# Performance work log

Measured on AMD Instinct MI355X. Metric: run time of the kernel, lower is better.

## Reference

```python
import jax, jax.numpy as jnp
import numpy as np

B, S, D, N, L, V = 4, 2048, 512, 16, 4, 256
EPS = 1e-5


def layernorm(x, g, b):
    m = x.mean(-1, keepdims=True)
    v = ((x - m) ** 2).mean(-1, keepdims=True)
    return (x - m) * jax.lax.rsqrt(v + EPS) * g + b


def ssm_layer(x, logA, Wd, bd, WB, bB, WC, bC, WDp, bDp, g, be):
    # x: (B,S,D)
    h = layernorm(x, g, be)
    delta = jax.nn.softplus(h @ Wd + bd)          # (B,S,D)
    Bi = h @ WB + bB                              # (B,S,N)
    Ci = h @ WC + bC                              # (B,S,N)
    A = -jnp.exp(logA)                            # (D,N)

    def step(state, inp):
        d_t, b_t, c_t, h_t = inp                  # (B,D),(B,N),(B,N),(B,D)
        dA = jnp.exp(d_t[:, :, None] * A)         # (B,D,N)
        state = dA * state + (d_t * h_t)[:, :, None] * b_t[:, None, :]
        y_t = jnp.einsum('bdn,bn->bd', state, c_t)
        return state, y_t

    xs = (jnp.moveaxis(delta, 1, 0), jnp.moveaxis(Bi, 1, 0),
          jnp.moveaxis(Ci, 1, 0), jnp.moveaxis(h, 1, 0))
    init = jnp.zeros((x.shape[0], x.shape[2], logA.shape[-1]), x.dtype)
    _, ys = jax.lax.scan(step, init, xs)
    y = jnp.moveaxis(ys, 0, 1)                    # (B,S,D)
    return x + y + h @ WDp + bDp


def setup_inputs() -> dict:
    key = jax.random.key(0)
    ks = jax.random.split(key, 12)
    s = 0.02
    byte_ids = jax.random.randint(ks[0], (B, S), 0, 256)
    emb_byte = jax.random.normal(ks[1], (V, D), jnp.float32) * s
    emb_pos = jax.random.normal(ks[2], (S, D), jnp.float32) * s
    logA = jnp.tile(jnp.log(jnp.linspace(1.0, N, N, dtype=jnp.float32)), (L, D, 1))
    Wd = jax.random.normal(ks[3], (L, D, D), jnp.float32) * s
    bd = jnp.zeros((L, D), jnp.float32)
    WB = jax.random.normal(ks[4], (L, D, N), jnp.float32) * s
    bB = jnp.zeros((L, N), jnp.float32)
    WC = jax.random.normal(ks[5], (L, D, N), jnp.float32) * s
    bC = jnp.zeros((L, N), jnp.float32)
    WDp = jax.random.normal(ks[6], (L, D, D), jnp.float32) * s
    bDp = jnp.zeros((L, D), jnp.float32)
    gamma = jnp.ones((L, D), jnp.float32)
    beta = jnp.zeros((L, D), jnp.float32)
    Wh = jax.random.normal(ks[7], (D, V), jnp.float32) * s
    bh = jnp.zeros((V,), jnp.float32)
    return {'byte_ids': byte_ids, 'emb_byte': emb_byte, 'emb_pos': emb_pos,
            'logA': logA, 'Wd': Wd, 'bd': bd, 'WB': WB, 'bB': bB,
            'WC': WC, 'bC': bC, 'WDp': WDp, 'bDp': bDp,
            'gamma': gamma, 'beta': beta, 'Wh': Wh, 'bh': bh}


def reference(byte_ids, emb_byte, emb_pos, logA, Wd, bd, WB, bB, WC, bC,
              WDp, bDp, gamma, beta, Wh, bh):
    S_ = byte_ids.shape[1]
    h = emb_byte[byte_ids] + emb_pos[:S_]
    for l in range(Wd.shape[0]):
        h = ssm_layer(h, logA[l], Wd[l], bd[l], WB[l], bB[l], WC[l], bC[l],
                      WDp[l], bDp[l], gamma[l], beta[l])
    return h @ Wh + bh                            # (B,S,256) logits
```

## Files before the change

kernel.cpp:

```cpp
#include <hip/hip_runtime.h>
#include <math.h>

#define BB 4
#define SS 2048
#define DD 512
#define NN 16
#define LL 4
#define VV 256
#define CC 64
#define TT (SS / CC)
#define EPSL 1e-5f
#define MM (BB * SS)
#define KI 16
#define LPAD 528

typedef __bf16 bf16;
typedef __attribute__((ext_vector_type(8))) __bf16 bf16x8;
typedef __attribute__((ext_vector_type(4))) __bf16 bf16x4;
typedef __attribute__((ext_vector_type(4))) float f32x4;


#define GLD_LDS(g, l) \
    __builtin_amdgcn_global_load_lds((__attribute__((address_space(1))) void*)(void*)(g), \
                                     (__attribute__((address_space(3))) void*)(l), 16, 0, 0)

__device__ __forceinline__ void ln_row_write(float4 v0, float4 v1, int lane, size_t row,
                                             const float* __restrict__ gamma,
                                             const float* __restrict__ beta,
                                             float* HN, bf16* HNb) {
    float s = v0.x + v0.y + v0.z + v0.w + v1.x + v1.y + v1.z + v1.w;
    float q = v0.x * v0.x + v0.y * v0.y + v0.z * v0.z + v0.w * v0.w +
              v1.x * v1.x + v1.y * v1.y + v1.z * v1.z + v1.w * v1.w;
#pragma unroll
    for (int o = 1; o < 64; o <<= 1) {
        s += __shfl_xor(s, o);
        q += __shfl_xor(q, o);
    }
    float m = s * (1.0f / DD);
    float var = q * (1.0f / DD) - m * m;
    float rs = rsqrtf(var + EPSL);
    float4 g0 = *(const float4*)(gamma + lane * 4);
    float4 g1 = *(const float4*)(gamma + 256 + lane * 4);
    float4 b0 = *(const float4*)(beta + lane * 4);
    float4 b1 = *(const float4*)(beta + 256 + lane * 4);
    float4 o0, o1;
    o0.x = (v0.x - m) * rs * g0.x + b0.x;
    o0.y = (v0.y - m) * rs * g0.y + b0.y;
    o0.z = (v0.z - m) * rs * g0.z + b0.z;
    o0.w = (v0.w - m) * rs * g0.w + b0.w;
    o1.x = (v1.x - m) * rs * g1.x + b1.x;
    o1.y = (v1.y - m) * rs * g1.y + b1.y;
    o1.z = (v1.z - m) * rs * g1.z + b1.z;
    o1.w = (v1.w - m) * rs * g1.w + b1.w;
    float* hr = HN + row * DD;
    *(float4*)(hr + lane * 4) = o0;
    *(float4*)(hr + 256 + lane * 4) = o1;
    size_t pb = (size_t)(row >> 4) * 8192 + (size_t)(lane >> 3) * 512 +
                (size_t)((lane & 7) >> 1) * 128 + (row & 15) * 8 + (lane & 1) * 4;
    bf16x4 p0 = {(bf16)o0.x, (bf16)o0.y, (bf16)o0.z, (bf16)o0.w};
    bf16x4 p1 = {(bf16)o1.x, (bf16)o1.y, (bf16)o1.z, (bf16)o1.w};
    *(bf16x4*)(HNb + pb) = p0;
    *(bf16x4*)(HNb + pb + 8 * 512) = p1;
}

__global__ void embed_ln(const int* __restrict__ ids,
                         const float* __restrict__ eb,
                         const float* __restrict__ ep,
                         const float* __restrict__ gamma,
                         const float* __restrict__ beta,
                         float* __restrict__ X, float* HN, bf16* HNb) {
    int wave = threadIdx.x >> 6;
    int lane = threadIdx.x & 63;
    size_t row = blockIdx.x * 4 + wave;
    int s = (int)(row & (SS - 1));
    int id = ids[row];
    const float* ebr = eb + (size_t)id * DD;
    const float* epr = ep + (size_t)s * DD;
    float4 e0 = *(const float4*)(ebr + lane * 4);
    float4 e1 = *(const float4*)(ebr + 256 + lane * 4);
    float4 p0 = *(const float4*)(epr + lane * 4);
    float4 p1 = *(const float4*)(epr + 256 + lane * 4);
    float4 v0 = {e0.x + p0.x, e0.y + p0.y, e0.z + p0.z, e0.w + p0.w};
    float4 v1 = {e1.x + p1.x, e1.y + p1.y, e1.z + p1.z, e1.w + p1.w};
    *(float4*)(X + row * DD + lane * 4) = v0;
    *(float4*)(X + row * DD + 256 + lane * 4) = v1;
    ln_row_write(v0, v1, lane, row, gamma, beta, HN, HNb);
}

__global__ __launch_bounds__(256) void convert_weights(const float* __restrict__ Wd,
                                                       const float* __restrict__ WDp,
                                                       const float* __restrict__ Wh,
                                                       bf16* __restrict__ WtP) {
    __shared__ float slab[512 * 17];
    int blk = blockIdx.x;
    const float* src;
    int nsrc, col0;
    bf16* dst;
    if (blk < 256) {
        int l = blk >> 6, tile = blk & 63;
        src = (tile < 32) ? (Wd + (size_t)l * DD * DD) : (WDp + (size_t)l * DD * DD);
        col0 = (tile & 31) * 16;
        nsrc = DD;
        dst = WtP + ((size_t)l * 64 + tile) * 8192;
    } else {
        int tile = blk - 256;
        src = Wh;
        col0 = tile * 16;
        nsrc = VV;
        dst = WtP + (size_t)(256 + tile) * 8192;
    }
    int tid = threadIdx.x;
    int kr = tid >> 2, cq = tid & 3;
#pragma unroll
    for (int i = 0; i < 8; i++) {
        int k = i * 64 + kr;
        float4 v = *(const float4*)(src + (size_t)k * nsrc + col0 + cq * 4);
        slab[k * 17 + cq * 4 + 0] = v.x;
        slab[k * 17 + cq * 4 + 1] = v.y;
        slab[k * 17 + cq * 4 + 2] = v.z;
        slab[k * 17 + cq * 4 + 3] = v.w;
    }
    __syncthreads();
#pragma unroll
    for (int it = 0; it < 4; it++) {
        int c = it * 256 + tid;
        int ki = c >> 6, fq = (c >> 4) & 3, fm = c & 15;
        int k0 = ki * 32 + fq * 8;
        bf16x8 v;
#pragma unroll
        for (int e = 0; e < 8; e++) v[e] = (bf16)slab[(k0 + e) * 17 + fm];
        *(bf16x8*)(dst + (size_t)c * 8) = v;
    }
}

template <int MODE, int NT>
__global__ __launch_bounds__(256, 8) void gemm_pack(const bf16* __restrict__ Ap,
                                                    const bf16* __restrict__ Bp,
                                                    const float* __restrict__ bias,
                                                    const float* __restrict__ bias2,
                                                    const float* __restrict__ Xres,
                                                    float* __restrict__ O1,
                                                    float* __restrict__ O2, int Nout) {
    __shared__ bf16 As[4 * 512];
    __shared__ bf16 Bs[4 * 512];
    const int tid = threadIdx.x, wave = tid >> 6, lane = tid & 63;
    const int lin = blockIdx.x;
    const int xcd = lin & 7, i4 = lin >> 3;
    const int ms = xcd * 16 + (i4 & 15);
    const int nb = i4 >> 4;

    const bf16* gA = Ap + ((size_t)ms * 4 + wave) * 8192 + lane * 8;
    const bf16* gB = Bp + ((size_t)nb * 4 + wave) * 8192 + lane * 8;
    bf16* lA = As + wave * 512;
    bf16* lB = Bs + wave * 512;

    const int fa0 = (wave >> 1) * 2, fb0 = (wave & 1) * 2;

    f32x4 acc[2][2];
#pragma unroll
    for (int i = 0; i < 2; i++)
#pragma unroll
        for (int j = 0; j < 2; j++) acc[i][j] = (f32x4){0.f, 0.f, 0.f, 0.f};

    for (int ki = 0; ki < KI; ki++) {
        GLD_LDS(gA + ki * 512, lA);
        GLD_LDS(gB + ki * 512, lB);
        __syncthreads();
        bf16x8 af[2], bfr[2];
#pragma unroll
        for (int i = 0; i < 2; i++) af[i] = *(const bf16x8*)(As + (fa0 + i) * 512 + lane * 8);
#pragma unroll
        for (int j = 0; j < 2; j++) bfr[j] = *(const bf16x8*)(Bs + (fb0 + j) * 512 + lane * 8);
#pragma unroll
        for (int i = 0; i < 2; i++)
#pragma unroll
            for (int j = 0; j < 2; j++)
                acc[i][j] = __builtin_amdgcn_mfma_f32_16x16x32_bf16(af[i], bfr[j], acc[i][j], 0, 0, 0);
        __syncthreads();
    }

    const int fm = lane & 15, fq = lane >> 4;
#pragma unroll
    for (int i = 0; i < 2; i++) {
#pragma unroll
        for (int j = 0; j < 2; j++) {
            int col = (nb * 4 + fb0 + j) * 16 + fm;
#pragma unroll
            for (int r = 0; r < 4; r++) {
                int row = (ms * 4 + fa0 + i) * 16 + fq * 4 + r;
                float v = acc[i][j][r];
                if (MODE == 0) {
                    O1[(size_t)row * Nout + col] = v + bias[col];
                } else {
                    if (col < DD) {
                        v += bias[col];
                        v = fmaxf(v, 0.0f) + log1pf(__expf(-fabsf(v)));
                        O1[(size_t)row * DD + col] = v;
                    } else {
                        int c = col - DD;
                        O2[(size_t)row * DD + c] = v + bias2[c] + Xres[(size_t)row * DD + c];
                    }
                }
            }
        }
    }
}

__global__ __launch_bounds__(512) void scan1bc(const float* __restrict__ DEL,
                                               const float* __restrict__ HN,
                                               const float* __restrict__ WB,
                                               const float* __restrict__ bB,
                                               const float* __restrict__ WC,
                                               const float* __restrict__ bC,
                                               const float* __restrict__ logA,
                                               float* __restrict__ P,
                                               float* __restrict__ LSt,
                                               float* __restrict__ BIo,
                                               float* __restrict__ CIo) {
    __shared__ float hn[32 * LPAD];
    __shared__ float bis[32 * 16], cis[32 * 16];
    int b = blockIdx.x / CC, c = blockIdx.x % CC;
    size_t row0 = (size_t)b * SS + c * TT;
    const float* hsrc = HN + row0 * DD;
    for (int v = threadIdx.x; v < 4096; v += 512) {
        int t = v >> 7, qd = v & 127;
        float4 x = *(const float4*)(hsrc + (size_t)t * DD + qd * 4);
        *(float4*)(hn + t * LPAD + qd * 4) = x;
    }
    __syncthreads();
    {
        int t = threadIdx.x >> 4, col = threadIdx.x & 15;
        float aB = 0.0f, aC = 0.0f;
        const float* hr = hn + t * LPAD;
#pragma unroll 8
        for (int k = 0; k < DD; k++) {
            float h = hr[k];
            aB = fmaf(h, WB[k * NN + col], aB);
            aC = fmaf(h, WC[k * NN + col], aC);
        }
        aB += bB[col];
        aC += bC[col];
        bis[threadIdx.x] = aB;
        cis[threadIdx.x] = aC;
        BIo[row0 * NN + threadIdx.x] = aB;
        CIo[row0 * NN + threadIdx.x] = aC;
    }
    __syncthreads();
    int d = threadIdx.x;
    float Ar[NN], prod[NN], st[NN];
#pragma unroll
    for (int n = 0; n < NN; n++) {
        Ar[n] = -__expf(logA[d * NN + n]);
        prod[n] = 1.0f;
        st[n] = 0.0f;
    }
    for (int tt = 0; tt < TT; tt++) {
        size_t base = row0 + tt;
        float dl = DEL[base * DD + d];
        float du = dl * hn[tt * LPAD + d];
#pragma unroll
        for (int n = 0; n < NN; n++) {
            float a = __expf(dl * Ar[n]);
            prod[n] *= a;
            st[n] = fmaf(a, st[n], du * bis[tt * 16 + n]);
        }
    }
    size_t o = (((size_t)b * DD + d) * CC + c) * NN;
#pragma unroll
    for (int n = 0; n < NN; n++) {
        P[o + n] = prod[n];
        LSt[o + n] = st[n];
    }
}

__global__ void scan2(const float* __restrict__ P, float* __restrict__ LS) {
    int tid = blockIdx.x * 256 + threadIdx.x;
    int n = tid & (NN - 1);
    int d = (tid / NN) & (DD - 1);
    int b = tid / (NN * DD);
    size_t base = ((size_t)b * DD + d) * CC;
    float s = 0.0f;
    for (int c = 0; c < CC; c++) {
        size_t o = base * NN + (size_t)c * NN + n;
        float p = P[o];
        float ls = LS[o];
        LS[o] = s;
        s = fmaf(p, s, ls);
    }
}

template <int LAST>
__global__ __launch_bounds__(512) void scan3ln(const float* __restrict__ DEL,
                                               float* HN,
                                               const float* __restrict__ BI,
                                               const float* __restrict__ CI,
                                               const float* __restrict__ logA,
                                               const float* __restrict__ SIN,
                                               const float* __restrict__ D2,
                                               const float* __restrict__ gamma,
                                               const float* __restrict__ beta,
                                               float* __restrict__ X,
                                               bf16* HNb) {
    __shared__ float xvs[32 * LPAD];
    int b = blockIdx.x / CC, c = blockIdx.x % CC;
    int d = threadIdx.x;
    float Ar[NN], st[NN];
    size_t o = (((size_t)b * DD + d) * CC + c) * NN;
#pragma unroll
    for (int n = 0; n < NN; n++) {
        Ar[n] = -__expf(logA[d * NN + n]);
        st[n] = SIN[o + n];
    }
    size_t row0 = (size_t)b * SS + c * TT;
    for (int tt = 0; tt < TT; tt++) {
        size_t base = row0 + tt;
        float dl = DEL[base * DD + d];
        float du = dl * HN[base * DD + d];
        const float* bi = BI + base * NN;
        const float* ci = CI + base * NN;
        float y = 0.0f;
#pragma unroll
        for (int n = 0; n < NN; n++) {
            float a = __expf(dl * Ar[n]);
            st[n] = fmaf(a, st[n], du * bi[n]);
            y = fmaf(st[n], ci[n], y);
        }
        float xv = D2[base * DD + d] + y;
        xvs[tt * LPAD + d] = xv;
        if (!LAST) X[base * DD + d] = xv;
    }
    __syncthreads();
    int wv = d >> 6, lane = d & 63;
#pragma unroll
    for (int r = 0; r < 4; r++) {
        int tt = wv * 4 + r;
        size_t row = row0 + tt;
        const float* xr = xvs + tt * LPAD;
        float4 v0 = *(const float4*)(xr + lane * 4);
        float4 v1 = *(const float4*)(xr + 256 + lane * 4);
        if (LAST) {
            size_t pb = (size_t)(row >> 4) * 8192 + (size_t)(lane >> 3) * 512 +
                        (size_t)((lane & 7) >> 1) * 128 + (row & 15) * 8 + (lane & 1) * 4;
            bf16x4 p0 = {(bf16)v0.x, (bf16)v0.y, (bf16)v0.z, (bf16)v0.w};
            bf16x4 p1 = {(bf16)v1.x, (bf16)v1.y, (bf16)v1.z, (bf16)v1.w};
            *(bf16x4*)(HNb + pb) = p0;
            *(bf16x4*)(HNb + pb + 8 * 512) = p1;
        } else {
            ln_row_write(v0, v1, lane, row, gamma, beta, HN, HNb);
        }
    }
}

extern "C" void kernel_launch(void* const* d_in, const int* in_sizes, int n_in,
                              void* d_out, int out_size, void* d_ws, size_t ws_size,
                              hipStream_t stream) {
    const int* ids = (const int*)d_in[0];
    const float* eb = (const float*)d_in[1];
    const float* ep = (const float*)d_in[2];
    const float* logA = (const float*)d_in[3];
    const float* Wd = (const float*)d_in[4];
    const float* bd = (const float*)d_in[5];
    const float* WB = (const float*)d_in[6];
    const float* bB = (const float*)d_in[7];
    const float* WC = (const float*)d_in[8];
    const float* bC = (const float*)d_in[9];
    const float* WDp = (const float*)d_in[10];
    const float* bDp = (const float*)d_in[11];
    const float* gamma = (const float*)d_in[12];
    const float* beta = (const float*)d_in[13];
    const float* Wh = (const float*)d_in[14];
    const float* bh = (const float*)d_in[15];
    float* out = (float*)d_out;

    size_t E = (size_t)MM * DD;
    size_t EN = (size_t)MM * NN;
    size_t EC = (size_t)BB * DD * CC * NN;
    float* X = (float*)d_ws;
    float* HN = X + E;
    float* DEL = HN + E;
    float* D2 = DEL + E;
    float* BIc = D2 + E;
    float* CIc = BIc + EN;
    float* P = CIc + EN;
    float* LS = P + EC;
    bf16* HNb = (bf16*)(LS + EC);
    bf16* WtP = HNb + E;

    embed_ln<<<MM / 4, 256, 0, stream>>>(ids, eb, ep, gamma, beta, X, HN, HNb);
    convert_weights<<<272, 256, 0, stream>>>(Wd, WDp, Wh, WtP);
    for (int l = 0; l < LL; l++) {
        const float* lA = logA + (size_t)l * DD * NN;
        gemm_pack<1, 16><<<2048, 256, 0, stream>>>(
            HNb, WtP + (size_t)l * 524288, bd + l * DD, bDp + l * DD, X, DEL, D2, 1024);
        scan1bc<<<BB * CC, 512, 0, stream>>>(DEL, HN, WB + (size_t)l * DD * NN, bB + l * NN,
                                             WC + (size_t)l * DD * NN, bC + l * NN, lA,
                                             P, LS, BIc, CIc);
        scan2<<<(BB * DD * NN) / 256, 256, 0, stream>>>(P, LS);
        if (l < LL - 1) {
            scan3ln<0><<<BB * CC, 512, 0, stream>>>(DEL, HN, BIc, CIc, lA, LS, D2,
                                                    gamma + (l + 1) * DD, beta + (l + 1) * DD,
                                                    X, HNb);
        } else {
            scan3ln<1><<<BB * CC, 512, 0, stream>>>(DEL, HN, BIc, CIc, lA, LS, D2,
                                                    nullptr, nullptr, X, HNb);
        }
    }
    gemm_pack<0, 4><<<512, 256, 0, stream>>>(
        HNb, WtP + (size_t)2097152, bh, nullptr, nullptr, out, nullptr, VV);
}
```

Baseline: 538.1 us.

## Split B/C projection into own kernel, double scan chunks, parallelize carry pass

The B/C projection moves out of the first scan kernel into a separate bcproj kernel that stages WB and WC in shared memory. The chunk count doubles to 128, so the scan kernels get more blocks and shorter serial loops. The chunk-state layout becomes chunk-major so P/LS can be written as vectors. scan2 becomes a two-level parallel prefix per (b,d) instead of one serial loop over chunks. Workspace is reused by aliasing P onto X and B/C onto the output buffer, which depends on X being fully consumed before scan1 writes P.

```diff
diff --git a/kernel.cpp b/kernel.cpp
--- a/kernel.cpp
+++ b/kernel.cpp
@@ -7,7 +7,7 @@
 #define NN 16
 #define LL 4
 #define VV 256
-#define CC 64
+#define CC 128
 #define TT (SS / CC)
 #define EPSL 1e-5f
 #define MM (BB * SS)
@@ -206,86 +206,143 @@
     }
 }
 
-__global__ __launch_bounds__(512) void scan1bc(const float* __restrict__ DEL,
-                                               const float* __restrict__ HN,
-                                               const float* __restrict__ WB,
-                                               const float* __restrict__ bB,
-                                               const float* __restrict__ WC,
-                                               const float* __restrict__ bC,
-                                               const float* __restrict__ logA,
-                                               float* __restrict__ P,
-                                               float* __restrict__ LSt,
-                                               float* __restrict__ BIo,
-                                               float* __restrict__ CIo) {
-    __shared__ float hn[32 * LPAD];
-    __shared__ float bis[32 * 16], cis[32 * 16];
-    int b = blockIdx.x / CC, c = blockIdx.x % CC;
-    size_t row0 = (size_t)b * SS + c * TT;
-    const float* hsrc = HN + row0 * DD;
-    for (int v = threadIdx.x; v < 4096; v += 512) {
-        int t = v >> 7, qd = v & 127;
-        float4 x = *(const float4*)(hsrc + (size_t)t * DD + qd * 4);
-        *(float4*)(hn + t * LPAD + qd * 4) = x;
-    }
-    __syncthreads();
-    {
-        int t = threadIdx.x >> 4, col = threadIdx.x & 15;
-        float aB = 0.0f, aC = 0.0f;
-        const float* hr = hn + t * LPAD;
-#pragma unroll 8
-        for (int k = 0; k < DD; k++) {
-            float h = hr[k];
-            aB = fmaf(h, WB[k * NN + col], aB);
-            aC = fmaf(h, WC[k * NN + col], aC);
-        }
-        aB += bB[col];
-        aC += bC[col];
-        bis[threadIdx.x] = aB;
-        cis[threadIdx.x] = aC;
-        BIo[row0 * NN + threadIdx.x] = aB;
-        CIo[row0 * NN + threadIdx.x] = aC;
-    }
-    __syncthreads();
+__global__ __launch_bounds__(256) void bcproj(const float* __restrict__ HN,
+                                              const float* __restrict__ WB,
+                                              const float* __restrict__ bB,
+                                              const float* __restrict__ WC,
+                                              const float* __restrict__ bC,
+                                              float* __restrict__ BIo,
+                                              float* __restrict__ CIo) {
+    __shared__ float W[512 * 32];
+    int tid = threadIdx.x;
+#pragma unroll
+    for (int i = 0; i < 8; i++) {
+        int f = i * 256 + tid;
+        int k = f >> 2, c4 = (f & 3) * 4;
+        float4 v = *(const float4*)(WB + (size_t)f * 4);
+        W[k * 32 + c4 + 0] = v.x;
+        W[k * 32 + c4 + 1] = v.y;
+        W[k * 32 + c4 + 2] = v.z;
+        W[k * 32 + c4 + 3] = v.w;
+        float4 u = *(const float4*)(WC + (size_t)f * 4);
+        W[k * 32 + 16 + c4 + 0] = u.x;
+        W[k * 32 + 16 + c4 + 1] = u.y;
+        W[k * 32 + 16 + c4 + 2] = u.z;
+        W[k * 32 + 16 + c4 + 3] = u.w;
+    }
+    __syncthreads();
+    int r = tid >> 5, c = tid & 31;
+    size_t row = (size_t)blockIdx.x * 8 + r;
+    const float* hr = HN + row * DD;
+    float acc0 = 0.0f, acc1 = 0.0f;
+#pragma unroll 4
+    for (int k = 0; k < DD; k += 8) {
+        float4 a0 = *(const float4*)(hr + k);
+        float4 a1 = *(const float4*)(hr + k + 4);
+        acc0 = fmaf(a0.x, W[(k + 0) * 32 + c], acc0);
+        acc1 = fmaf(a0.y, W[(k + 1) * 32 + c], acc1);
+        acc0 = fmaf(a0.z, W[(k + 2) * 32 + c], acc0);
+        acc1 = fmaf(a0.w, W[(k + 3) * 32 + c], acc1);
+        acc0 = fmaf(a1.x, W[(k + 4) * 32 + c], acc0);
+        acc1 = fmaf(a1.y, W[(k + 5) * 32 + c], acc1);
+        acc0 = fmaf(a1.z, W[(k + 6) * 32 + c], acc0);
+        acc1 = fmaf(a1.w, W[(k + 7) * 32 + c], acc1);
+    }
+    float acc = acc0 + acc1;
+    if (c < NN) BIo[row * NN + c] = acc + bB[c];
+    else        CIo[row * NN + (c - NN)] = acc + bC[c - NN];
+}
+
+__global__ __launch_bounds__(512) void scan1(const float* __restrict__ DEL,
+                                             const float* __restrict__ HN,
+                                             const float* __restrict__ BIc,
+                                             const float* __restrict__ logA,
+                                             float* __restrict__ P,
+                                             float* __restrict__ LSt) {
+    __shared__ float bis[TT * NN];
+    int b = blockIdx.x >> 7, c = blockIdx.x & (CC - 1);
     int d = threadIdx.x;
+    size_t row0 = (size_t)b * SS + (size_t)c * TT;
+    if (d < TT * NN) bis[d] = BIc[row0 * NN + d];
     float Ar[NN], prod[NN], st[NN];
+    const float* la = logA + d * NN;
+#pragma unroll
+    for (int n = 0; n < NN; n += 4) {
+        float4 a4 = *(const float4*)(la + n);
+        Ar[n + 0] = -__expf(a4.x);
+        Ar[n + 1] = -__expf(a4.y);
+        Ar[n + 2] = -__expf(a4.z);
+        Ar[n + 3] = -__expf(a4.w);
+    }
 #pragma unroll
     for (int n = 0; n < NN; n++) {
-        Ar[n] = -__expf(logA[d * NN + n]);
         prod[n] = 1.0f;
         st[n] = 0.0f;
     }
+    __syncthreads();
+    const float* dp = DEL + row0 * DD + d;
+    const float* hp = HN + row0 * DD + d;
+#pragma unroll 4
     for (int tt = 0; tt < TT; tt++) {
-        size_t base = row0 + tt;
-        float dl = DEL[base * DD + d];
-        float du = dl * hn[tt * LPAD + d];
+        float dl = dp[(size_t)tt * DD];
+        float du = dl * hp[(size_t)tt * DD];
 #pragma unroll
         for (int n = 0; n < NN; n++) {
             float a = __expf(dl * Ar[n]);
             prod[n] *= a;
-            st[n] = fmaf(a, st[n], du * bis[tt * 16 + n]);
-        }
-    }
-    size_t o = (((size_t)b * DD + d) * CC + c) * NN;
-#pragma unroll
-    for (int n = 0; n < NN; n++) {
-        P[o + n] = prod[n];
-        LSt[o + n] = st[n];
-    }
-}
-
-__global__ void scan2(const float* __restrict__ P, float* __restrict__ LS) {
-    int tid = blockIdx.x * 256 + threadIdx.x;
-    int n = tid & (NN - 1);
-    int d = (tid / NN) & (DD - 1);
-    int b = tid / (NN * DD);
-    size_t base = ((size_t)b * DD + d) * CC;
-    float s = 0.0f;
-    for (int c = 0; c < CC; c++) {
-        size_t o = base * NN + (size_t)c * NN + n;
-        float p = P[o];
-        float ls = LS[o];
+            st[n] = fmaf(a, st[n], du * bis[tt * NN + n]);
+        }
+    }
+    size_t o = (((size_t)b * CC + c) * DD + d) * NN;
+#pragma unroll
+    for (int n = 0; n < NN; n += 4) {
+        *(f32x4*)(P + o + n) = (f32x4){prod[n], prod[n + 1], prod[n + 2], prod[n + 3]};
+        *(f32x4*)(LSt + o + n) = (f32x4){st[n], st[n + 1], st[n + 2], st[n + 3]};
+    }
+}
+
+__global__ __launch_bounds__(256) void scan2(const float* __restrict__ P,
+                                             float* __restrict__ LS) {
+    __shared__ float sP[256], sL[256];
+    int bd = blockIdx.x;
+    int b = bd >> 9, d = bd & (DD - 1);
+    int n = threadIdx.x & (NN - 1), g = threadIdx.x >> 4;
+    size_t base = ((size_t)b * CC * DD + d) * NN + n;
+    const size_t cs = (size_t)DD * NN;
+    float p[8], l[8];
+#pragma unroll
+    for (int i = 0; i < 8; i++) {
+        size_t o = base + (size_t)(g * 8 + i) * cs;
+        p[i] = P[o];
+        l[i] = LS[o];
+    }
+    float FP = 1.0f, FL = 0.0f;
+#pragma unroll
+    for (int i = 0; i < 8; i++) {
+        FL = fmaf(p[i], FL, l[i]);
+        FP *= p[i];
+    }
+    sP[threadIdx.x] = FP;
+    sL[threadIdx.x] = FL;
+    __syncthreads();
+    if (threadIdx.x < NN) {
+        int nn = threadIdx.x;
+        float s = 0.0f;
+#pragma unroll
+        for (int gg = 0; gg < 16; gg++) {
+            float fp = sP[gg * 16 + nn];
+            float fl = sL[gg * 16 + nn];
+            sL[gg * 16 + nn] = s;
+            s = fmaf(fp, s, fl);
+        }
+    }
+    __syncthreads();
+    float s = sL[g * 16 + n];
+#pragma unroll
+    for (int i = 0; i < 8; i++) {
+        size_t o = base + (size_t)(g * 8 + i) * cs;
         LS[o] = s;
-        s = fmaf(p, s, ls);
+        s = fmaf(p[i], s, l[i]);
     }
 }
 
@@ -301,39 +358,56 @@
                                                const float* __restrict__ beta,
                                                float* __restrict__ X,
                                                bf16* HNb) {
-    __shared__ float xvs[32 * LPAD];
-    int b = blockIdx.x / CC, c = blockIdx.x % CC;
+    __shared__ float xvs[TT * LPAD];
+    __shared__ float bis[TT * NN], cis[TT * NN];
+    int b = blockIdx.x >> 7, c = blockIdx.x & (CC - 1);
     int d = threadIdx.x;
+    size_t row0 = (size_t)b * SS + (size_t)c * TT;
+    if (d < TT * NN) {
+        bis[d] = BI[row0 * NN + d];
+        cis[d] = CI[row0 * NN + d];
+    }
     float Ar[NN], st[NN];
-    size_t o = (((size_t)b * DD + d) * CC + c) * NN;
-#pragma unroll
-    for (int n = 0; n < NN; n++) {
-        Ar[n] = -__expf(logA[d * NN + n]);
-        st[n] = SIN[o + n];
-    }
-    size_t row0 = (size_t)b * SS + c * TT;
+    size_t o = (((size_t)b * CC + c) * DD + d) * NN;
+    const float* la = logA + d * NN;
+#pragma unroll
+    for (int n = 0; n < NN; n += 4) {
+        float4 a4 = *(const float4*)(la + n);
+        Ar[n + 0] = -__expf(a4.x);
+        Ar[n + 1] = -__expf(a4.y);
+        Ar[n + 2] = -__expf(a4.z);
+        Ar[n + 3] = -__expf(a4.w);
+        float4 s4 = *(const float4*)(SIN + o + n);
+        st[n + 0] = s4.x;
+        st[n + 1] = s4.y;
+        st[n + 2] = s4.z;
+        st[n + 3] = s4.w;
+    }
+    __syncthreads();
+    const float* dp = DEL + row0 * DD + d;
+    const float* hp = HN + row0 * DD + d;
+    const float* d2p = D2 + row0 * DD + d;
+    float* xp = X + row0 * DD + d;
+#pragma unroll 4
     for (int tt = 0; tt < TT; tt++) {
-        size_t base = row0 + tt;
-        float dl = DEL[base * DD + d];
-        float du = dl * HN[base * DD + d];
-        const float* bi = BI + base * NN;
-        const float* ci = CI + base * NN;
+        float dl = dp[(size_t)tt * DD];
+        float du = dl * hp[(size_t)tt * DD];
         float y = 0.0f;
 #pragma unroll
         for (int n = 0; n < NN; n++) {
             float a = __expf(dl * Ar[n]);
-            st[n] = fmaf(a, st[n], du * bi[n]);
-            y = fmaf(st[n], ci[n], y);
-        }
-        float xv = D2[base * DD + d] + y;
+            st[n] = fmaf(a, st[n], du * bis[tt * NN + n]);
+            y = fmaf(st[n], cis[tt * NN + n], y);
+        }
+        float xv = d2p[(size_t)tt * DD] + y;
         xvs[tt * LPAD + d] = xv;
-        if (!LAST) X[base * DD + d] = xv;
+        if (!LAST) xp[(size_t)tt * DD] = xv;
     }
     __syncthreads();
     int wv = d >> 6, lane = d & 63;
 #pragma unroll
-    for (int r = 0; r < 4; r++) {
-        int tt = wv * 4 + r;
+    for (int r = 0; r < 2; r++) {
+        int tt = wv * 2 + r;
         size_t row = row0 + tt;
         const float* xr = xvs + tt * LPAD;
         float4 v0 = *(const float4*)(xr + lane * 4);
@@ -374,28 +448,28 @@
 
     size_t E = (size_t)MM * DD;
     size_t EN = (size_t)MM * NN;
-    size_t EC = (size_t)BB * DD * CC * NN;
     float* X = (float*)d_ws;
     float* HN = X + E;
     float* DEL = HN + E;
     float* D2 = DEL + E;
-    float* BIc = D2 + E;
-    float* CIc = BIc + EN;
-    float* P = CIc + EN;
-    float* LS = P + EC;
-    bf16* HNb = (bf16*)(LS + EC);
+    float* LS = D2 + E;
+    bf16* HNb = (bf16*)(LS + E);
     bf16* WtP = HNb + E;
+    float* P = X;
+    float* BIc = out;
+    float* CIc = out + EN;
 
     embed_ln<<<MM / 4, 256, 0, stream>>>(ids, eb, ep, gamma, beta, X, HN, HNb);
     convert_weights<<<272, 256, 0, stream>>>(Wd, WDp, Wh, WtP);
     for (int l = 0; l < LL; l++) {
         const float* lA = logA + (size_t)l * DD * NN;
+        bcproj<<<MM / 8, 256, 0, stream>>>(HN, WB + (size_t)l * DD * NN, bB + l * NN,
+                                           WC + (size_t)l * DD * NN, bC + l * NN,
+                                           BIc, CIc);
         gemm_pack<1, 16><<<2048, 256, 0, stream>>>(
             HNb, WtP + (size_t)l * 524288, bd + l * DD, bDp + l * DD, X, DEL, D2, 1024);
-        scan1bc<<<BB * CC, 512, 0, stream>>>(DEL, HN, WB + (size_t)l * DD * NN, bB + l * NN,
-                                             WC + (size_t)l * DD * NN, bC + l * NN, lA,
-                                             P, LS, BIc, CIc);
-        scan2<<<(BB * DD * NN) / 256, 256, 0, stream>>>(P, LS);
+        scan1<<<BB * CC, 512, 0, stream>>>(DEL, HN, BIc, lA, P, LS);
+        scan2<<<BB * DD, 256, 0, stream>>>(P, LS);
         if (l < LL - 1) {
             scan3ln<0><<<BB * CC, 512, 0, stream>>>(DEL, HN, BIc, CIc, lA, LS, D2,
                                                     gamma + (l + 1) * DD, beta + (l + 1) * DD,
```

New measurement: 544.8 us. No clear change (+1.3%).
